# Kernel optimization log

Hardware: AMD Instinct MI355X
Metric: run time of the kernel (lower is better)

Reference implementation:

```python
import jax, jax.numpy as jnp
import numpy as np

D_IN = 256
DIMS = 256


def setup_inputs() -> dict:
    key = jax.random.key(0)
    k1, k2, k3, k4, k5 = jax.random.split(key, 5)
    B, Tq, Tk = 4, 512, 512
    query = jax.random.normal(k1, (B, Tq, D_IN), dtype=jnp.float32)
    value = jax.random.normal(k2, (B, Tk, D_IN), dtype=jnp.float32)
    # Dense(dims, use_bias=False) kernels (glorot-like scale) and AdditiveAttention scale vector
    Wq = jax.random.normal(k3, (D_IN, DIMS), dtype=jnp.float32) / np.sqrt(D_IN)
    Wv = jax.random.normal(k4, (D_IN, DIMS), dtype=jnp.float32) / np.sqrt(D_IN)
    scale = jax.random.normal(k5, (DIMS,), dtype=jnp.float32)
    return {"query": query, "value": value, "Wq": Wq, "Wv": Wv, "scale": scale}


def reference(query, value, Wq, Wv, scale):
    # q_proj: [B,Tq,d], k_proj: [B,Tk,d]; attention value = RAW value tensor (as in source)
    q = jnp.einsum("bqi,id->bqd", query, Wq)
    k = jnp.einsum("bki,id->bkd", value, Wv)
    # Additive (Bahdanau) scores: [B,Tq,Tk] via broadcast tanh then reduce with scale
    scores = jnp.einsum("bqkd,d->bqk", jnp.tanh(q[:, :, None, :] + k[:, None, :, :]), scale)
    attn = jax.nn.softmax(scores, axis=-1)  # masks are all-ones -> no-op
    out = jnp.einsum("bqk,bki->bqi", attn, value)
    return out, attn
```

## Files before the change

kernel.cpp:

```cpp
#include <hip/hip_runtime.h>

#define LOG2E 1.4426950408889634f
#define TWO_LOG2E 2.885390081777927f

__device__ __forceinline__ float fast_exp2(float x) { return __builtin_amdgcn_exp2f(x); }
__device__ __forceinline__ float fast_rcp(float x)  { return __builtin_amdgcn_rcpf(x); }

__device__ __forceinline__ void term2(float s0, float s1, float qx, float qy,
                                      float kx, float ky, float& acc) {
    const float A = fmaf(qx, kx, 1.f);
    const float B = fmaf(qy, ky, 1.f);
    acc = fmaf(fmaf(s1, A, s0 * B), fast_rcp(A * B), acc);
}

__global__ __launch_bounds__(256) void proj_kernel(
    const float* __restrict__ query, const float* __restrict__ value,
    const float* __restrict__ Wq, const float* __restrict__ Wv,
    float* __restrict__ eq, float* __restrict__ ekT)
{
    __shared__ float in_lds[8 * 256];
    __shared__ float v_lds[64 * 68];
    __shared__ float w_lds[64 * 36];
    __shared__ float t_lds[32 * 68];

    const int t = threadIdx.x;
    const int bx = blockIdx.x;

    if (bx < 256) {
        const int row0 = bx * 8;
        const float4* s4 = (const float4*)(query + (size_t)row0 * 256);
        float4* l4 = (float4*)in_lds;
        l4[t] = s4[t];
        l4[t + 256] = s4[t + 256];
        __syncthreads();

        float acc[8];
#pragma unroll
        for (int r = 0; r < 8; ++r) acc[r] = 0.f;

        for (int d = 0; d < 256; d += 4) {
            const float w0 = Wq[(d + 0) * 256 + t];
            const float w1 = Wq[(d + 1) * 256 + t];
            const float w2 = Wq[(d + 2) * 256 + t];
            const float w3 = Wq[(d + 3) * 256 + t];
#pragma unroll
            for (int r = 0; r < 8; ++r) {
                const float4 v = *(const float4*)&in_lds[r * 256 + d];
                acc[r] = fmaf(v.x, w0, acc[r]);
                acc[r] = fmaf(v.y, w1, acc[r]);
                acc[r] = fmaf(v.z, w2, acc[r]);
                acc[r] = fmaf(v.w, w3, acc[r]);
            }
        }
        float* dst = eq + (size_t)row0 * 256;
#pragma unroll
        for (int r = 0; r < 8; ++r) dst[r * 256 + t] = fast_exp2(acc[r] * TWO_LOG2E);
    } else {
        const int bi = bx - 256;
        const int kt = bi >> 3, dt = bi & 7;
        const int gk0 = kt * 64;
        const int bb = gk0 >> 9, kin0 = gk0 & 511;
        const int dout0 = dt * 32;
        const int kp = t >> 3, dg = t & 7;

        float acc[2][4];
#pragma unroll
        for (int i = 0; i < 2; ++i)
#pragma unroll
            for (int j = 0; j < 4; ++j) acc[i][j] = 0.f;

        for (int dc = 0; dc < 256; dc += 64) {
            __syncthreads();
#pragma unroll
            for (int l = 0; l < 4; ++l) {
                const int idx = t + 256 * l;
                const int r = idx >> 4, c4 = (idx & 15) * 4;
                *(float4*)&v_lds[r * 68 + c4] =
                    *(const float4*)&value[(size_t)(gk0 + r) * 256 + dc + c4];
            }
#pragma unroll
            for (int l = 0; l < 2; ++l) {
                const int idx = t + 256 * l;
                const int r = idx >> 3, c4 = (idx & 7) * 4;
                *(float4*)&w_lds[r * 36 + c4] =
                    *(const float4*)&Wv[(size_t)(dc + r) * 256 + dout0 + c4];
            }
            __syncthreads();

#pragma unroll 8
            for (int din = 0; din < 64; ++din) {
                const float v0 = v_lds[(2 * kp + 0) * 68 + din];
                const float v1 = v_lds[(2 * kp + 1) * 68 + din];
                const float4 wv = *(const float4*)&w_lds[din * 36 + 4 * dg];
                acc[0][0] = fmaf(v0, wv.x, acc[0][0]);
                acc[0][1] = fmaf(v0, wv.y, acc[0][1]);
                acc[0][2] = fmaf(v0, wv.z, acc[0][2]);
                acc[0][3] = fmaf(v0, wv.w, acc[0][3]);
                acc[1][0] = fmaf(v1, wv.x, acc[1][0]);
                acc[1][1] = fmaf(v1, wv.y, acc[1][1]);
                acc[1][2] = fmaf(v1, wv.z, acc[1][2]);
                acc[1][3] = fmaf(v1, wv.w, acc[1][3]);
            }
        }
        __syncthreads();
#pragma unroll
        for (int i = 0; i < 2; ++i)
#pragma unroll
            for (int j = 0; j < 4; ++j)
                t_lds[(4 * dg + j) * 68 + 2 * kp + i] =
                    fast_exp2(acc[i][j] * TWO_LOG2E);
        __syncthreads();
#pragma unroll
        for (int l = 0; l < 2; ++l) {
            const int idx = t + 256 * l;
            const int row = idx >> 4, c4 = (idx & 15) * 4;
            *(float4*)&ekT[(size_t)bb * 131072 + (size_t)(dout0 + row) * 512 + kin0 + c4] =
                *(const float4*)&t_lds[row * 68 + c4];
        }
    }
}

#define EQ_ST 260
#define SS_ST 520
__global__ __launch_bounds__(256, 3) void fused_kernel(
    const float* __restrict__ eq, const float* __restrict__ ekT,
    const float* __restrict__ scale, const float* __restrict__ value,
    float* __restrict__ attn, float* __restrict__ out)
{
    __shared__ float eq_lds[4 * EQ_ST];
    __shared__ float sc_lds[256];
    __shared__ float s_tile[4 * SS_ST];
    __shared__ float red[2 * 4 * 256];
    __shared__ float inv_lds[4];

    const int t = threadIdx.x;
    const int w = t >> 6, lane = t & 63;
    const int kg = (w << 6) + lane;
    const int k0 = 2 * kg;
    const int qt = blockIdx.x, b = blockIdx.y;
    const int q0 = qt * 4;

    {
        const float4 v = ((const float4*)(eq + (size_t)(b * 512 + q0) * 256))[t];
        const int row = t >> 6, c = t & 63;
        *(float4*)&eq_lds[row * EQ_ST + 4 * c] = v;
    }
    sc_lds[t] = -2.f * scale[t];
    __syncthreads();

    const float* ekTb = ekT + (size_t)b * 131072 + k0;
    const float* q0r = &eq_lds[0 * EQ_ST];
    const float* q1r = &eq_lds[1 * EQ_ST];
    const float* q2r = &eq_lds[2 * EQ_ST];
    const float* q3r = &eq_lds[3 * EQ_ST];

    float a00 = 0.f, a01 = 0.f, a10 = 0.f, a11 = 0.f;
    float a20 = 0.f, a21 = 0.f, a30 = 0.f, a31 = 0.f;

    float4 sv  = *(const float4*)&sc_lds[0];
    float4 qv0 = *(const float4*)&q0r[0];
    float4 qv1 = *(const float4*)&q1r[0];
    float4 qv2 = *(const float4*)&q2r[0];
    float4 qv3 = *(const float4*)&q3r[0];
    float2 k0v = *(const float2*)&ekTb[(size_t)0 * 512];
    float2 k1v = *(const float2*)&ekTb[(size_t)1 * 512];
    float2 k2v = *(const float2*)&ekTb[(size_t)2 * 512];
    float2 k3v = *(const float2*)&ekTb[(size_t)3 * 512];

#pragma unroll 4
    for (int d = 0; d < 256; d += 4) {
        const float4 csv = sv, c0 = qv0, c1 = qv1, c2 = qv2, c3 = qv3;
        const float2 ck0 = k0v, ck1 = k1v, ck2 = k2v, ck3 = k3v;

        if (d < 252) {
            const int dn = d + 4;
            sv  = *(const float4*)&sc_lds[dn];
            qv0 = *(const float4*)&q0r[dn];
            qv1 = *(const float4*)&q1r[dn];
            qv2 = *(const float4*)&q2r[dn];
            qv3 = *(const float4*)&q3r[dn];
            k0v = *(const float2*)&ekTb[(size_t)(dn + 0) * 512];
            k1v = *(const float2*)&ekTb[(size_t)(dn + 1) * 512];
            k2v = *(const float2*)&ekTb[(size_t)(dn + 2) * 512];
            k3v = *(const float2*)&ekTb[(size_t)(dn + 3) * 512];
        }

        term2(csv.x, csv.y, c0.x, c0.y, ck0.x, ck1.x, a00);
        term2(csv.z, csv.w, c0.z, c0.w, ck2.x, ck3.x, a00);
        term2(csv.x, csv.y, c0.x, c0.y, ck0.y, ck1.y, a01);
        term2(csv.z, csv.w, c0.z, c0.w, ck2.y, ck3.y, a01);

        term2(csv.x, csv.y, c1.x, c1.y, ck0.x, ck1.x, a10);
        term2(csv.z, csv.w, c1.z, c1.w, ck2.x, ck3.x, a10);
        term2(csv.x, csv.y, c1.x, c1.y, ck0.y, ck1.y, a11);
        term2(csv.z, csv.w, c1.z, c1.w, ck2.y, ck3.y, a11);

        term2(csv.x, csv.y, c2.x, c2.y, ck0.x, ck1.x, a20);
        term2(csv.z, csv.w, c2.z, c2.w, ck2.x, ck3.x, a20);
        term2(csv.x, csv.y, c2.x, c2.y, ck0.y, ck1.y, a21);
        term2(csv.z, csv.w, c2.z, c2.w, ck2.y, ck3.y, a21);

        term2(csv.x, csv.y, c3.x, c3.y, ck0.x, ck1.x, a30);
        term2(csv.z, csv.w, c3.z, c3.w, ck2.x, ck3.x, a30);
        term2(csv.x, csv.y, c3.x, c3.y, ck0.y, ck1.y, a31);
        term2(csv.z, csv.w, c3.z, c3.w, ck2.y, ck3.y, a31);
    }

    *(float2*)&s_tile[0 * SS_ST + k0] = make_float2(a00, a01);
    *(float2*)&s_tile[1 * SS_ST + k0] = make_float2(a10, a11);
    *(float2*)&s_tile[2 * SS_ST + k0] = make_float2(a20, a21);
    *(float2*)&s_tile[3 * SS_ST + k0] = make_float2(a30, a31);
    __syncthreads();

    {
        float x[8];
        float m = -1e30f;
#pragma unroll
        for (int j = 0; j < 8; ++j) {
            x[j] = s_tile[w * SS_ST + 64 * j + lane];
            m = fmaxf(m, x[j]);
        }
#pragma unroll
        for (int off = 32; off; off >>= 1) m = fmaxf(m, __shfl_xor(m, off));

        float sum = 0.f;
#pragma unroll
        for (int j = 0; j < 8; ++j) { x[j] = fast_exp2((x[j] - m) * LOG2E); sum += x[j]; }
#pragma unroll
        for (int off = 32; off; off >>= 1) sum += __shfl_xor(sum, off);
        const float inv = fast_rcp(sum);

        float* arow = attn + (size_t)(b * 512 + q0 + w) * 512;
#pragma unroll
        for (int j = 0; j < 8; ++j) {
            s_tile[w * SS_ST + 64 * j + lane] = x[j];
            arow[64 * j + lane] = x[j] * inv;
        }
        if (lane == 0) inv_lds[w] = inv;
    }
    __syncthreads();

    float4 acc[4];
#pragma unroll
    for (int r = 0; r < 4; ++r) acc[r] = make_float4(0.f, 0.f, 0.f, 0.f);

    const float* vbase = value + (size_t)(b * 512 + 128 * w) * 256;
    for (int k4 = 0; k4 < 128; k4 += 4) {
        const float4 v0 = *(const float4*)&vbase[(k4 + 0) * 256 + lane * 4];
        const float4 v1 = *(const float4*)&vbase[(k4 + 1) * 256 + lane * 4];
        const float4 v2 = *(const float4*)&vbase[(k4 + 2) * 256 + lane * 4];
        const float4 v3 = *(const float4*)&vbase[(k4 + 3) * 256 + lane * 4];
#pragma unroll
        for (int r = 0; r < 4; ++r) {
            const float4 s4 = *(const float4*)&s_tile[r * SS_ST + 128 * w + k4];
            acc[r].x = fmaf(s4.x, v0.x, acc[r].x); acc[r].y = fmaf(s4.x, v0.y, acc[r].y);
            acc[r].z = fmaf(s4.x, v0.z, acc[r].z); acc[r].w = fmaf(s4.x, v0.w, acc[r].w);
            acc[r].x = fmaf(s4.y, v1.x, acc[r].x); acc[r].y = fmaf(s4.y, v1.y, acc[r].y);
            acc[r].z = fmaf(s4.y, v1.z, acc[r].z); acc[r].w = fmaf(s4.y, v1.w, acc[r].w);
            acc[r].x = fmaf(s4.z, v2.x, acc[r].x); acc[r].y = fmaf(s4.z, v2.y, acc[r].y);
            acc[r].z = fmaf(s4.z, v2.z, acc[r].z); acc[r].w = fmaf(s4.z, v2.w, acc[r].w);
            acc[r].x = fmaf(s4.w, v3.x, acc[r].x); acc[r].y = fmaf(s4.w, v3.y, acc[r].y);
            acc[r].z = fmaf(s4.w, v3.z, acc[r].z); acc[r].w = fmaf(s4.w, v3.w, acc[r].w);
        }
    }

    if (w >= 2) {
#pragma unroll
        for (int r = 0; r < 4; ++r)
            *(float4*)&red[((w - 2) * 4 + r) * 256 + lane * 4] = acc[r];
    }
    __syncthreads();
    if (w < 2) {
#pragma unroll
        for (int r = 0; r < 4; ++r) {
            const float4 o = *(const float4*)&red[(w * 4 + r) * 256 + lane * 4];
            acc[r].x += o.x; acc[r].y += o.y; acc[r].z += o.z; acc[r].w += o.w;
        }
    }
    __syncthreads();
    if (w == 1) {
#pragma unroll
        for (int r = 0; r < 4; ++r)
            *(float4*)&red[r * 256 + lane * 4] = acc[r];
    }
    __syncthreads();
    if (w == 0) {
#pragma unroll
        for (int r = 0; r < 4; ++r) {
            const float4 o = *(const float4*)&red[r * 256 + lane * 4];
            const float iv = inv_lds[r];
            float4 res;
            res.x = (acc[r].x + o.x) * iv;
            res.y = (acc[r].y + o.y) * iv;
            res.z = (acc[r].z + o.z) * iv;
            res.w = (acc[r].w + o.w) * iv;
            *(float4*)&out[(size_t)(b * 512 + q0 + r) * 256 + lane * 4] = res;
        }
    }
}

extern "C" void kernel_launch(void* const* d_in, const int* in_sizes, int n_in,
                              void* d_out, int out_size, void* d_ws, size_t ws_size,
                              hipStream_t stream) {
    const float* query = (const float*)d_in[0];
    const float* value = (const float*)d_in[1];
    const float* Wq    = (const float*)d_in[2];
    const float* Wv    = (const float*)d_in[3];
    const float* scale = (const float*)d_in[4];

    float* out0 = (float*)d_out;
    float* attn = out0 + 4 * 512 * 256;

    float* eq  = (float*)d_ws;
    float* ekT = eq + 2048 * 256;

    proj_kernel<<<512, 256, 0, stream>>>(query, value, Wq, Wv, eq, ekT);
    fused_kernel<<<dim3(128, 4), 256, 0, stream>>>(eq, ekT, scale, value, attn, out0);
}
```

Before: 65.10 us.

## Double fused kernel block to 512 threads, splitting query rows across wave groups

The fused attention kernel now runs 512 threads per block. Each half of the block computes scores for two of the four query rows, so every thread holds fewer accumulators. The attn-times-value stage splits the key range across 8 waves instead of 4, with an extra LDS reduction step. This is meant to raise parallelism and latency hiding in the tanh-score loop, at the cost of each ekT load being fetched by two wave groups, more barriers and a larger reduction buffer.

```diff
diff --git a/kernel.cpp b/kernel.cpp
--- a/kernel.cpp
+++ b/kernel.cpp
@@ -122,7 +122,7 @@
 
 #define EQ_ST 260
 #define SS_ST 520
-__global__ __launch_bounds__(256, 3) void fused_kernel(
+__global__ __launch_bounds__(512, 2) void fused_kernel(
     const float* __restrict__ eq, const float* __restrict__ ekT,
     const float* __restrict__ scale, const float* __restrict__ value,
     float* __restrict__ attn, float* __restrict__ out)
@@ -130,38 +130,35 @@
     __shared__ float eq_lds[4 * EQ_ST];
     __shared__ float sc_lds[256];
     __shared__ float s_tile[4 * SS_ST];
-    __shared__ float red[2 * 4 * 256];
+    __shared__ float red[4 * 4 * 256];
     __shared__ float inv_lds[4];
 
     const int t = threadIdx.x;
     const int w = t >> 6, lane = t & 63;
-    const int kg = (w << 6) + lane;
+    const int qg = w >> 2;
+    const int kg = ((w & 3) << 6) + lane;
     const int k0 = 2 * kg;
     const int qt = blockIdx.x, b = blockIdx.y;
     const int q0 = qt * 4;
 
-    {
+    if (t < 256) {
         const float4 v = ((const float4*)(eq + (size_t)(b * 512 + q0) * 256))[t];
         const int row = t >> 6, c = t & 63;
         *(float4*)&eq_lds[row * EQ_ST + 4 * c] = v;
-    }
-    sc_lds[t] = -2.f * scale[t];
+    } else {
+        sc_lds[t - 256] = -2.f * scale[t - 256];
+    }
     __syncthreads();
 
     const float* ekTb = ekT + (size_t)b * 131072 + k0;
-    const float* q0r = &eq_lds[0 * EQ_ST];
-    const float* q1r = &eq_lds[1 * EQ_ST];
-    const float* q2r = &eq_lds[2 * EQ_ST];
-    const float* q3r = &eq_lds[3 * EQ_ST];
+    const float* q0r = &eq_lds[(2 * qg + 0) * EQ_ST];
+    const float* q1r = &eq_lds[(2 * qg + 1) * EQ_ST];
 
     float a00 = 0.f, a01 = 0.f, a10 = 0.f, a11 = 0.f;
-    float a20 = 0.f, a21 = 0.f, a30 = 0.f, a31 = 0.f;
 
     float4 sv  = *(const float4*)&sc_lds[0];
     float4 qv0 = *(const float4*)&q0r[0];
     float4 qv1 = *(const float4*)&q1r[0];
-    float4 qv2 = *(const float4*)&q2r[0];
-    float4 qv3 = *(const float4*)&q3r[0];
     float2 k0v = *(const float2*)&ekTb[(size_t)0 * 512];
     float2 k1v = *(const float2*)&ekTb[(size_t)1 * 512];
     float2 k2v = *(const float2*)&ekTb[(size_t)2 * 512];
@@ -169,7 +166,7 @@
 
 #pragma unroll 4
     for (int d = 0; d < 256; d += 4) {
-        const float4 csv = sv, c0 = qv0, c1 = qv1, c2 = qv2, c3 = qv3;
+        const float4 csv = sv, c0 = qv0, c1 = qv1;
         const float2 ck0 = k0v, ck1 = k1v, ck2 = k2v, ck3 = k3v;
 
         if (d < 252) {
@@ -177,8 +174,6 @@
             sv  = *(const float4*)&sc_lds[dn];
             qv0 = *(const float4*)&q0r[dn];
             qv1 = *(const float4*)&q1r[dn];
-            qv2 = *(const float4*)&q2r[dn];
-            qv3 = *(const float4*)&q3r[dn];
             k0v = *(const float2*)&ekTb[(size_t)(dn + 0) * 512];
             k1v = *(const float2*)&ekTb[(size_t)(dn + 1) * 512];
             k2v = *(const float2*)&ekTb[(size_t)(dn + 2) * 512];
@@ -194,25 +189,13 @@
         term2(csv.z, csv.w, c1.z, c1.w, ck2.x, ck3.x, a10);
         term2(csv.x, csv.y, c1.x, c1.y, ck0.y, ck1.y, a11);
         term2(csv.z, csv.w, c1.z, c1.w, ck2.y, ck3.y, a11);
-
-        term2(csv.x, csv.y, c2.x, c2.y, ck0.x, ck1.x, a20);
-        term2(csv.z, csv.w, c2.z, c2.w, ck2.x, ck3.x, a20);
-        term2(csv.x, csv.y, c2.x, c2.y, ck0.y, ck1.y, a21);
-        term2(csv.z, csv.w, c2.z, c2.w, ck2.y, ck3.y, a21);
-
-        term2(csv.x, csv.y, c3.x, c3.y, ck0.x, ck1.x, a30);
-        term2(csv.z, csv.w, c3.z, c3.w, ck2.x, ck3.x, a30);
-        term2(csv.x, csv.y, c3.x, c3.y, ck0.y, ck1.y, a31);
-        term2(csv.z, csv.w, c3.z, c3.w, ck2.y, ck3.y, a31);
-    }
-
-    *(float2*)&s_tile[0 * SS_ST + k0] = make_float2(a00, a01);
-    *(float2*)&s_tile[1 * SS_ST + k0] = make_float2(a10, a11);
-    *(float2*)&s_tile[2 * SS_ST + k0] = make_float2(a20, a21);
-    *(float2*)&s_tile[3 * SS_ST + k0] = make_float2(a30, a31);
-    __syncthreads();
-
-    {
+    }
+
+    *(float2*)&s_tile[(2 * qg + 0) * SS_ST + k0] = make_float2(a00, a01);
+    *(float2*)&s_tile[(2 * qg + 1) * SS_ST + k0] = make_float2(a10, a11);
+    __syncthreads();
+
+    if (w < 4) {
         float x[8];
         float m = -1e30f;
 #pragma unroll
@@ -244,15 +227,15 @@
 #pragma unroll
     for (int r = 0; r < 4; ++r) acc[r] = make_float4(0.f, 0.f, 0.f, 0.f);
 
-    const float* vbase = value + (size_t)(b * 512 + 128 * w) * 256;
-    for (int k4 = 0; k4 < 128; k4 += 4) {
+    const float* vbase = value + (size_t)(b * 512 + 64 * w) * 256;
+    for (int k4 = 0; k4 < 64; k4 += 4) {
         const float4 v0 = *(const float4*)&vbase[(k4 + 0) * 256 + lane * 4];
         const float4 v1 = *(const float4*)&vbase[(k4 + 1) * 256 + lane * 4];
         const float4 v2 = *(const float4*)&vbase[(k4 + 2) * 256 + lane * 4];
         const float4 v3 = *(const float4*)&vbase[(k4 + 3) * 256 + lane * 4];
 #pragma unroll
         for (int r = 0; r < 4; ++r) {
-            const float4 s4 = *(const float4*)&s_tile[r * SS_ST + 128 * w + k4];
+            const float4 s4 = *(const float4*)&s_tile[r * SS_ST + 64 * w + k4];
             acc[r].x = fmaf(s4.x, v0.x, acc[r].x); acc[r].y = fmaf(s4.x, v0.y, acc[r].y);
             acc[r].z = fmaf(s4.x, v0.z, acc[r].z); acc[r].w = fmaf(s4.x, v0.w, acc[r].w);
             acc[r].x = fmaf(s4.y, v1.x, acc[r].x); acc[r].y = fmaf(s4.y, v1.y, acc[r].y);
@@ -264,7 +247,21 @@
         }
     }
 
-    if (w >= 2) {
+    if (w >= 4) {
+#pragma unroll
+        for (int r = 0; r < 4; ++r)
+            *(float4*)&red[((w - 4) * 4 + r) * 256 + lane * 4] = acc[r];
+    }
+    __syncthreads();
+    if (w < 4) {
+#pragma unroll
+        for (int r = 0; r < 4; ++r) {
+            const float4 o = *(const float4*)&red[(w * 4 + r) * 256 + lane * 4];
+            acc[r].x += o.x; acc[r].y += o.y; acc[r].z += o.z; acc[r].w += o.w;
+        }
+    }
+    __syncthreads();
+    if (w >= 2 && w < 4) {
 #pragma unroll
         for (int r = 0; r < 4; ++r)
             *(float4*)&red[((w - 2) * 4 + r) * 256 + lane * 4] = acc[r];
@@ -315,5 +312,5 @@
     float* ekT = eq + 2048 * 256;
 
     proj_kernel<<<512, 256, 0, stream>>>(query, value, Wq, Wv, eq, ekT);
-    fused_kernel<<<dim3(128, 4), 256, 0, stream>>>(eq, ekT, scale, value, attn, out0);
+    fused_kernel<<<dim3(128, 4), 512, 0, stream>>>(eq, ekT, scale, value, attn, out0);
 }
```

Result: slower. 70.33 us (+8.0%).
